# Kernel optimization log

Measured on AMD Instinct MI355X. Metric: run time of the kernel, lower is better.

Reference implementation:

```python
import jax, jax.numpy as jnp
import numpy as np

B, CIN, COUT, K, KN, HID, HW = 16, 256, 256, 3, 4, 16, 64
PAD = K // 2
EPS = 1e-5


def setup_inputs() -> dict:
    key = jax.random.key(0)
    ks = jax.random.split(key, 6)
    x = jax.random.normal(ks[0], (B, CIN, HW, HW), dtype=jnp.float32)
    # attention MLP: 1x1 conv -> BN -> ReLU -> 1x1 conv (on 1x1 pooled maps == dense)
    w1 = jax.random.normal(ks[1], (HID, CIN), dtype=jnp.float32) * (1.0 / np.sqrt(CIN))
    bn_gamma = jnp.ones((HID,), dtype=jnp.float32)
    bn_beta = jnp.zeros((HID,), dtype=jnp.float32)
    bn_mean = jnp.zeros((HID,), dtype=jnp.float32)
    bn_var = jnp.ones((HID,), dtype=jnp.float32)
    w2 = jax.random.normal(ks[2], (KN, HID), dtype=jnp.float32) * (1.0 / np.sqrt(HID))
    # kaiming-normal fan_out: std = sqrt(2 / (Cout * k * k))
    weight = jax.random.normal(ks[3], (KN, COUT, CIN, K, K), dtype=jnp.float32) * np.sqrt(2.0 / (COUT * K * K))
    return {"x": x, "w1": w1, "bn_gamma": bn_gamma, "bn_beta": bn_beta,
            "bn_mean": bn_mean, "bn_var": bn_var, "w2": w2, "weight": weight}


def reference(x, w1, bn_gamma, bn_beta, bn_mean, bn_var, w2, weight):
    b = x.shape[0]
    # global average pool -> [B, Cin]
    pooled = jnp.mean(x, axis=(2, 3))
    h = pooled @ w1.T                                   # [B, HID]
    h = (h - bn_mean) * jax.lax.rsqrt(bn_var + EPS) * bn_gamma + bn_beta
    h = jax.nn.relu(h)
    att = jax.nn.softmax(h @ w2.T, axis=1)              # [B, KN]
    # aggregate per-sample kernels: [B, Cout, Cin, K, K]
    agg_w = jnp.einsum('bk,koijl->boijl', att, weight)
    # batched dynamic conv via batch-as-groups grouped conv
    x_g = x.reshape(1, b * CIN, x.shape[2], x.shape[3])
    w_g = agg_w.reshape(b * COUT, CIN, K, K)
    out = jax.lax.conv_general_dilated(
        x_g, w_g, window_strides=(1, 1), padding=[(PAD, PAD), (PAD, PAD)],
        dimension_numbers=('NCHW', 'OIHW', 'NCHW'), feature_group_count=b)
    return out.reshape(b, COUT, out.shape[2], out.shape[3])
```

## Files before the change

kernel.cpp:

```cpp
#include <hip/hip_runtime.h>

typedef __attribute__((ext_vector_type(8))) short bf16x8;
typedef __attribute__((ext_vector_type(4))) float f32x4;

#define AS3 __attribute__((address_space(3)))
#define AS1 __attribute__((address_space(1)))

__device__ __forceinline__ unsigned short f2bf(float f) {
  unsigned u = __float_as_uint(f);
  u += 0x7fffu + ((u >> 16) & 1u);
  return (unsigned short)(u >> 16);
}

__global__ void pool_kernel(const float* __restrict__ x, float* __restrict__ pooled) {
  const int bc = blockIdx.x;
  const float4* p = reinterpret_cast<const float4*>(x) + (size_t)bc * 1024;
  float s = 0.f;
  for (int i = threadIdx.x; i < 1024; i += 256) {
    float4 v = p[i];
    s += v.x + v.y + v.z + v.w;
  }
#pragma unroll
  for (int off = 32; off > 0; off >>= 1) s += __shfl_xor(s, off, 64);
  __shared__ float wsum[4];
  if ((threadIdx.x & 63) == 0) wsum[threadIdx.x >> 6] = s;
  __syncthreads();
  if (threadIdx.x == 0)
    pooled[bc] = (wsum[0] + wsum[1] + wsum[2] + wsum[3]) * (1.0f / 4096.0f);
}

__global__ void transpose_kernel(const float* __restrict__ x,
                                 unsigned short* __restrict__ xTp) {
  __shared__ unsigned short tb[64][258];
  const int blk = blockIdx.x;
  const int b = blk >> 6, y = blk & 63;
  const int t = threadIdx.x;
  const int l = t & 63, w = t >> 6;
  const int coff = l >> 4;
  const int x4 = (l & 15) << 2;
  const float* src = x + (size_t)b * 256 * 4096 + (size_t)y * 64;
#pragma unroll 4
  for (int i = 0; i < 16; ++i) {
    const int c = w * 64 + i * 4 + coff;
    const float4 v = *reinterpret_cast<const float4*>(&src[(size_t)c * 4096 + x4]);
    tb[x4 + 0][c] = f2bf(v.x);
    tb[x4 + 1][c] = f2bf(v.y);
    tb[x4 + 2][c] = f2bf(v.z);
    tb[x4 + 3][c] = f2bf(v.w);
  }
  __syncthreads();
  unsigned short* dst = xTp + (size_t)b * (4356 * 256) + ((size_t)(y + 1) * 66 + 1) * 256;
#pragma unroll 4
  for (int i = 0; i < 16; ++i) {
    const int xx = w * 16 + i;
    ushort2 v0 = *(const ushort2*)&tb[xx][l * 4];
    ushort2 v1 = *(const ushort2*)&tb[xx][l * 4 + 2];
    ushort4 v = {v0.x, v0.y, v1.x, v1.y};
    *(ushort4*)&dst[(size_t)xx * 256 + l * 4] = v;
  }
}

__global__ void border_kernel(unsigned short* __restrict__ xTp) {
  const int br = blockIdx.x;
  const int b = blockIdx.y;
  int y, xx;
  if (br < 66) { y = 0; xx = br; }
  else if (br < 132) { y = 65; xx = br - 66; }
  else { const int k = br - 132; y = 1 + (k >> 1); xx = (k & 1) * 65; }
  xTp[((size_t)b * 4356 + y * 66 + xx) * 256 + threadIdx.x] = 0;
}

__global__ void attn_kernel(const float* __restrict__ pooled,
                            const float* __restrict__ w1,
                            const float* __restrict__ bng,
                            const float* __restrict__ bnb,
                            const float* __restrict__ bnm,
                            const float* __restrict__ bnv,
                            const float* __restrict__ w2,
                            float* __restrict__ att) {
  __shared__ float hbuf[256];
  const int t = threadIdx.x;
  const int b = t >> 4, i = t & 15;
  float s = 0.f;
  for (int c = 0; c < 256; ++c) s += pooled[b * 256 + c] * w1[i * 256 + c];
  float h = (s - bnm[i]) * rsqrtf(bnv[i] + 1e-5f) * bng[i] + bnb[i];
  hbuf[t] = fmaxf(h, 0.f);
  __syncthreads();
  if (t < 64) {
    const int bb = t >> 2, k = t & 3;
    float l = 0.f;
    for (int j = 0; j < 16; ++j) l += hbuf[bb * 16 + j] * w2[k * 16 + j];
    float m = l;
    m = fmaxf(m, __shfl_xor(m, 1, 64));
    m = fmaxf(m, __shfl_xor(m, 2, 64));
    float e = expf(l - m);
    float sum = e;
    sum += __shfl_xor(sum, 1, 64);
    sum += __shfl_xor(sum, 2, 64);
    att[bb * 4 + k] = e / sum;
  }
}

__global__ void agg_kernel(const float* __restrict__ att,
                           const float* __restrict__ wgt,
                           unsigned short* __restrict__ agg) {
  const int o = blockIdx.x;
  const int bh = blockIdx.y;
  const int c = threadIdx.x;
  float w[4][9];
#pragma unroll
  for (int k = 0; k < 4; ++k) {
    const float* wp = wgt + ((size_t)((k << 8) + o) * 256 + c) * 9;
#pragma unroll
    for (int t = 0; t < 9; ++t) w[k][t] = wp[t];
  }
  __shared__ float attS[64];
  if (c < 64) attS[c] = att[c];
  __syncthreads();
#pragma unroll 1
  for (int b = bh * 8; b < bh * 8 + 8; ++b) {
    const float a0 = attS[b * 4 + 0], a1 = attS[b * 4 + 1];
    const float a2 = attS[b * 4 + 2], a3 = attS[b * 4 + 3];
#pragma unroll
    for (int t = 0; t < 9; ++t) {
      const float v = a0 * w[0][t] + a1 * w[1][t] + a2 * w[2][t] + a3 * w[3][t];
      agg[(((size_t)(b * 9 + t) * 256) + o) * 256 + c] = f2bf(v);
    }
  }
}

__global__ __launch_bounds__(512, 4) void conv_kernel(
    const unsigned short* __restrict__ xTp,
    const unsigned short* __restrict__ agg,
    float* __restrict__ out) {
  __shared__ unsigned short lds[512 * 32 + 4 * 128 * 32];
  AS3 char* ldsA3 = (AS3 char*)lds;
  AS3 char* ldsB3 = (AS3 char*)(lds + 512 * 32);

  const int bid = blockIdx.x;
  const int b = bid & 15;
  const int rest = bid >> 4;
  const int mt = rest >> 1;
  const int nh = rest & 1;
  const int p0 = mt << 8;
  const int rowA0 = mt * 264;

  const int tid = threadIdx.x;
  const int lane = tid & 63;
  const int wave = tid >> 6;
  const int wm = wave >> 1;
  const int wn = wave & 1;

  const int srow = tid >> 2;
  const int scol = ((tid & 3) ^ ((tid >> 3) & 3)) << 3;
  const int sdst = srow * 64 + (tid & 3) * 16;

  const unsigned short* xbs =
      xTp + (size_t)b * (4356 * 256) + (size_t)rowA0 * 256 + scol;
  const unsigned short* aggs =
      agg + ((size_t)(b * 9) * 256 + nh * 128 + srow) * 256 + scol;

  auto stageA = [&](int c0) {
#pragma unroll
    for (int i = 0; i < 4; ++i) {
      const int h = srow + (i << 7);
      const int hs = h > 395 ? 395 : h;
      __builtin_amdgcn_global_load_lds(
          (const AS1 void*)(xbs + (size_t)hs * 256 + c0 * 32),
          (AS3 void*)(ldsA3 + sdst + (i << 13)), 16, 0, 0);
    }
  };
  auto stageB = [&](int c02, int tap2, int slot) {
    __builtin_amdgcn_global_load_lds(
        (const AS1 void*)(aggs + tap2 * 65536 + c02 * 32),
        (AS3 void*)(ldsB3 + slot * 8192 + sdst), 16, 0, 0);
  };

  const int l15 = lane & 15;
  const int lhi = lane >> 4;
  const int hb = wm * 66 + l15;
  const int rslotB = (lhi ^ ((l15 >> 1) & 3)) << 4;
  int boffs[4];
#pragma unroll
  for (int n = 0; n < 4; ++n)
    boffs[n] = 32768 + (wn * 64 + n * 16 + l15) * 64 + rslotB;

  f32x4 acc[4][4];
#pragma unroll
  for (int m = 0; m < 4; ++m)
#pragma unroll
    for (int n = 0; n < 4; ++n) acc[m][n] = (f32x4){0.f, 0.f, 0.f, 0.f};

  stageB(0, 0, 0);
  stageB(0, 1, 1);

#pragma unroll 1
  for (int c0 = 0; c0 < 8; ++c0) {
    __builtin_amdgcn_s_barrier();
    stageA(c0);
    asm volatile("s_waitcnt vmcnt(0)" ::: "memory");
    __builtin_amdgcn_s_barrier();
#pragma unroll
    for (int tap = 0; tap < 9; ++tap) {
      if (tap != 0) {
        asm volatile("s_waitcnt vmcnt(1)" ::: "memory");
        __builtin_amdgcn_s_barrier();
      }
      __builtin_amdgcn_sched_barrier(0);
      const int dy = tap / 3, dx = tap % 3;
      const int slotR = (c0 + tap) & 3;
      bf16x8 af[4], bfr[4];
#pragma unroll
      for (int m = 0; m < 4; ++m) {
        const int h = hb + dy * 66 + dx + m * 16;
        const int ab = h * 64 + ((lhi ^ ((h >> 1) & 3)) << 4);
        af[m] = *(const bf16x8*)((const char*)lds + ab);
      }
#pragma unroll
      for (int n = 0; n < 4; ++n)
        bfr[n] = *(const bf16x8*)((const char*)lds + slotR * 8192 + boffs[n]);
      int c02, tap2;
      if (tap <= 6) { c02 = c0; tap2 = tap + 2; }
      else { c02 = c0 + 1; tap2 = tap - 7; }
      if (c02 > 7) { c02 = 7; tap2 = 8; }
      stageB(c02, tap2, (c0 + tap + 2) & 3);
      __builtin_amdgcn_s_setprio(1);
#pragma unroll
      for (int m = 0; m < 4; ++m)
#pragma unroll
        for (int n = 0; n < 4; ++n)
          acc[m][n] = __builtin_amdgcn_mfma_f32_16x16x32_bf16(af[m], bfr[n],
                                                              acc[m][n], 0, 0, 0);
      __builtin_amdgcn_s_setprio(0);
    }
  }

#pragma unroll
  for (int m = 0; m < 4; ++m) {
    const int p = p0 + wm * 64 + m * 16 + (lhi << 2);
#pragma unroll
    for (int n = 0; n < 4; ++n) {
      const int co = nh * 128 + wn * 64 + n * 16 + l15;
      float* dst = out + ((size_t)(b * 256 + co) << 12) + p;
      *reinterpret_cast<f32x4*>(dst) = acc[m][n];
    }
  }
}

extern "C" void kernel_launch(void* const* d_in, const int* in_sizes, int n_in,
                              void* d_out, int out_size, void* d_ws, size_t ws_size,
                              hipStream_t stream) {
  const float* x = (const float*)d_in[0];
  const float* w1 = (const float*)d_in[1];
  const float* bng = (const float*)d_in[2];
  const float* bnb = (const float*)d_in[3];
  const float* bnm = (const float*)d_in[4];
  const float* bnv = (const float*)d_in[5];
  const float* w2 = (const float*)d_in[6];
  const float* wgt = (const float*)d_in[7];
  float* out = (float*)d_out;

  char* ws = (char*)d_ws;
  const size_t xtp_bytes = (size_t)16 * 4356 * 256 * 2;
  const size_t agg_bytes = (size_t)16 * 9 * 256 * 256 * 2;
  unsigned short* xTp = (unsigned short*)ws;
  unsigned short* agg = (unsigned short*)(ws + xtp_bytes);
  float* pooled = (float*)(ws + xtp_bytes + agg_bytes);
  float* att = (float*)(ws + xtp_bytes + agg_bytes + 16384);

  border_kernel<<<dim3(260, 16), 256, 0, stream>>>(xTp);
  transpose_kernel<<<1024, 256, 0, stream>>>(x, xTp);
  pool_kernel<<<4096, 256, 0, stream>>>(x, pooled);
  attn_kernel<<<1, 256, 0, stream>>>(pooled, w1, bng, bnb, bnm, bnv, w2, att);
  agg_kernel<<<dim3(256, 2), 256, 0, stream>>>(att, wgt, agg);
  conv_kernel<<<512, 512, 0, stream>>>(xTp, agg, out);
}
```

Measured before the change: 122.0 us.

## Halve conv workgroup to 4 waves with 8x4 MFMA tiles; pool from bf16 transpose

```diff
diff --git a/kernel.cpp b/kernel.cpp
--- a/kernel.cpp
+++ b/kernel.cpp
@@ -11,22 +11,8 @@
   u += 0x7fffu + ((u >> 16) & 1u);
   return (unsigned short)(u >> 16);
 }
-
-__global__ void pool_kernel(const float* __restrict__ x, float* __restrict__ pooled) {
-  const int bc = blockIdx.x;
-  const float4* p = reinterpret_cast<const float4*>(x) + (size_t)bc * 1024;
-  float s = 0.f;
-  for (int i = threadIdx.x; i < 1024; i += 256) {
-    float4 v = p[i];
-    s += v.x + v.y + v.z + v.w;
-  }
-#pragma unroll
-  for (int off = 32; off > 0; off >>= 1) s += __shfl_xor(s, off, 64);
-  __shared__ float wsum[4];
-  if ((threadIdx.x & 63) == 0) wsum[threadIdx.x >> 6] = s;
-  __syncthreads();
-  if (threadIdx.x == 0)
-    pooled[bc] = (wsum[0] + wsum[1] + wsum[2] + wsum[3]) * (1.0f / 4096.0f);
+__device__ __forceinline__ float bf2f(unsigned short v) {
+  return __uint_as_float((unsigned)v << 16);
 }
 
 __global__ void transpose_kernel(const float* __restrict__ x,
@@ -70,6 +56,37 @@
   xTp[((size_t)b * 4356 + y * 66 + xx) * 256 + threadIdx.x] = 0;
 }
 
+__global__ void pool2_kernel(const unsigned short* __restrict__ xTp,
+                             float* __restrict__ pooled) {
+  __shared__ float red[8][256];
+  const int b = blockIdx.x;
+  const int ych = blockIdx.y;
+  const int t = threadIdx.x;
+  const int rg = t >> 5;
+  const int c8 = (t & 31) << 3;
+  const unsigned short* base = xTp + (size_t)b * (4356 * 256);
+  float s[8];
+#pragma unroll
+  for (int k = 0; k < 8; ++k) s[k] = 0.f;
+  for (int rr = 0; rr < 32; ++rr) {
+    const int r = rr * 8 + rg;
+    const int y = ych * 4 + (r >> 6);
+    const int xx = r & 63;
+    const unsigned short* row =
+        base + ((size_t)(y + 1) * 66 + 1 + xx) * 256 + c8;
+    bf16x8 v = *reinterpret_cast<const bf16x8*>(row);
+#pragma unroll
+    for (int k = 0; k < 8; ++k) s[k] += bf2f((unsigned short)v[k]);
+  }
+#pragma unroll
+  for (int k = 0; k < 8; ++k) red[rg][c8 + k] = s[k];
+  __syncthreads();
+  float tot = 0.f;
+#pragma unroll
+  for (int g = 0; g < 8; ++g) tot += red[g][t];
+  atomicAdd(&pooled[b * 256 + t], tot * (1.0f / 4096.0f));
+}
+
 __global__ void attn_kernel(const float* __restrict__ pooled,
                             const float* __restrict__ w1,
                             const float* __restrict__ bng,
@@ -129,13 +146,13 @@
   }
 }
 
-__global__ __launch_bounds__(512, 4) void conv_kernel(
+__global__ __launch_bounds__(256, 2) void conv_kernel(
     const unsigned short* __restrict__ xTp,
     const unsigned short* __restrict__ agg,
     float* __restrict__ out) {
-  __shared__ unsigned short lds[512 * 32 + 4 * 128 * 32];
+  __shared__ unsigned short lds[448 * 32 + 4 * 128 * 32];
   AS3 char* ldsA3 = (AS3 char*)lds;
-  AS3 char* ldsB3 = (AS3 char*)(lds + 512 * 32);
+  AS3 char* ldsB3 = ((AS3 char*)lds) + 28672;
 
   const int bid = blockIdx.x;
   const int b = bid & 15;
@@ -162,32 +179,35 @@
 
   auto stageA = [&](int c0) {
 #pragma unroll
-    for (int i = 0; i < 4; ++i) {
-      const int h = srow + (i << 7);
+    for (int i = 0; i < 7; ++i) {
+      const int h = srow + (i << 6);
       const int hs = h > 395 ? 395 : h;
       __builtin_amdgcn_global_load_lds(
           (const AS1 void*)(xbs + (size_t)hs * 256 + c0 * 32),
-          (AS3 void*)(ldsA3 + sdst + (i << 13)), 16, 0, 0);
+          (AS3 void*)(ldsA3 + sdst + (i << 12)), 16, 0, 0);
     }
   };
   auto stageB = [&](int c02, int tap2, int slot) {
-    __builtin_amdgcn_global_load_lds(
-        (const AS1 void*)(aggs + tap2 * 65536 + c02 * 32),
-        (AS3 void*)(ldsB3 + slot * 8192 + sdst), 16, 0, 0);
+#pragma unroll
+    for (int j = 0; j < 2; ++j) {
+      __builtin_amdgcn_global_load_lds(
+          (const AS1 void*)(aggs + tap2 * 65536 + (j << 14) + c02 * 32),
+          (AS3 void*)(ldsB3 + slot * 8192 + sdst + (j << 12)), 16, 0, 0);
+    }
   };
 
   const int l15 = lane & 15;
   const int lhi = lane >> 4;
-  const int hb = wm * 66 + l15;
+  const int hb0 = wm * 132 + l15;
   const int rslotB = (lhi ^ ((l15 >> 1) & 3)) << 4;
   int boffs[4];
 #pragma unroll
   for (int n = 0; n < 4; ++n)
-    boffs[n] = 32768 + (wn * 64 + n * 16 + l15) * 64 + rslotB;
-
-  f32x4 acc[4][4];
-#pragma unroll
-  for (int m = 0; m < 4; ++m)
+    boffs[n] = 28672 + (wn * 64 + n * 16 + l15) * 64 + rslotB;
+
+  f32x4 acc[8][4];
+#pragma unroll
+  for (int m = 0; m < 8; ++m)
 #pragma unroll
     for (int n = 0; n < 4; ++n) acc[m][n] = (f32x4){0.f, 0.f, 0.f, 0.f};
 
@@ -203,16 +223,16 @@
 #pragma unroll
     for (int tap = 0; tap < 9; ++tap) {
       if (tap != 0) {
-        asm volatile("s_waitcnt vmcnt(1)" ::: "memory");
+        asm volatile("s_waitcnt vmcnt(2)" ::: "memory");
         __builtin_amdgcn_s_barrier();
       }
       __builtin_amdgcn_sched_barrier(0);
       const int dy = tap / 3, dx = tap % 3;
       const int slotR = (c0 + tap) & 3;
-      bf16x8 af[4], bfr[4];
-#pragma unroll
-      for (int m = 0; m < 4; ++m) {
-        const int h = hb + dy * 66 + dx + m * 16;
+      bf16x8 af[8], bfr[4];
+#pragma unroll
+      for (int m = 0; m < 8; ++m) {
+        const int h = hb0 + ((m >> 2) + dy) * 66 + (m & 3) * 16 + dx;
         const int ab = h * 64 + ((lhi ^ ((h >> 1) & 3)) << 4);
         af[m] = *(const bf16x8*)((const char*)lds + ab);
       }
@@ -226,7 +246,7 @@
       stageB(c02, tap2, (c0 + tap + 2) & 3);
       __builtin_amdgcn_s_setprio(1);
 #pragma unroll
-      for (int m = 0; m < 4; ++m)
+      for (int m = 0; m < 8; ++m)
 #pragma unroll
         for (int n = 0; n < 4; ++n)
           acc[m][n] = __builtin_amdgcn_mfma_f32_16x16x32_bf16(af[m], bfr[n],
@@ -236,8 +256,8 @@
   }
 
 #pragma unroll
-  for (int m = 0; m < 4; ++m) {
-    const int p = p0 + wm * 64 + m * 16 + (lhi << 2);
+  for (int m = 0; m < 8; ++m) {
+    const int p = p0 + wm * 128 + (m >> 2) * 64 + (m & 3) * 16 + (lhi << 2);
 #pragma unroll
     for (int n = 0; n < 4; ++n) {
       const int co = nh * 128 + wn * 64 + n * 16 + l15;
@@ -268,10 +288,11 @@
   float* pooled = (float*)(ws + xtp_bytes + agg_bytes);
   float* att = (float*)(ws + xtp_bytes + agg_bytes + 16384);
 
+  hipMemsetAsync(pooled, 0, 16 * 256 * sizeof(float), stream);
   border_kernel<<<dim3(260, 16), 256, 0, stream>>>(xTp);
   transpose_kernel<<<1024, 256, 0, stream>>>(x, xTp);
-  pool_kernel<<<4096, 256, 0, stream>>>(x, pooled);
+  pool2_kernel<<<dim3(16, 16), 256, 0, stream>>>(xTp, pooled);
   attn_kernel<<<1, 256, 0, stream>>>(pooled, w1, bng, bnb, bnm, bnv, w2, att);
   agg_kernel<<<dim3(256, 2), 256, 0, stream>>>(att, wgt, agg);
-  conv_kernel<<<512, 512, 0, stream>>>(xTp, agg, out);
-}
+  conv_kernel<<<512, 256, 0, stream>>>(xTp, agg, out);
+}
```

Result: no change. 121.2 us (-0.7%).
